# Performance work log

Measured on AMD Instinct MI355X. Metric: run time of the kernel, lower is better.

## Reference

```python
import jax, jax.numpy as jnp
import numpy as np

BUCKETS = 32
DIM = 1024
HEADS = 16
TEMP = 0.75
SINK_ITERS = 7
LOG_EPS = 1e-6
GUMBEL_EPS = 1e-4


def _sinkhorn(r, n_iters):
    # iterative row/col log-normalization, then exp (matches torch loop)
    for _ in range(n_iters):
        r = r - jax.scipy.special.logsumexp(r, axis=2, keepdims=True)
        r = r - jax.scipy.special.logsumexp(r, axis=1, keepdims=True)
    return jnp.exp(r)


def setup_inputs() -> dict:
    key = jax.random.key(0)
    kq, kk, kv, kw, kg = jax.random.split(key, 5)
    B, H, T, DH = 4, 16, 4096, 64
    q = jax.random.normal(kq, (B, H, T, DH), jnp.float32)
    k = jax.random.normal(kk, (B, H, T, DH), jnp.float32)
    v = jax.random.normal(kv, (B, H, T, DH), jnp.float32)
    sort_w = jax.random.normal(kw, (1, H, DH, BUCKETS), jnp.float32)
    u = jax.random.uniform(kg, (B * H, BUCKETS, BUCKETS), jnp.float32, 0.0, 1.0)
    gumbel_noise = -jnp.log(-jnp.log(u + GUMBEL_EPS) + GUMBEL_EPS)
    return {"q": q, "k": k, "v": v, "sort_w": sort_w, "gumbel_noise": gumbel_noise}


def reference(q, k, v, sort_w, gumbel_noise):
    b, h, t, dh = q.shape
    bh = b * h
    bsz = t // BUCKETS  # tokens per bucket
    # bucket: (bh, buckets, bsz, dh)
    qb = q.reshape(bh, BUCKETS, bsz, dh)
    kb = k.reshape(bh, BUCKETS, bsz, dh)
    vb = v.reshape(bh, BUCKETS, bsz, dh)
    # bucket summaries for routing
    b_k_r = kb.sum(axis=2)  # (bh, buckets, dh)
    e_w = jnp.broadcast_to(sort_w, (b, h, dh, BUCKETS)).reshape(bh, dh, BUCKETS)
    R = jnp.log(jax.nn.relu(jnp.einsum('bud,bdv->buv', b_k_r, e_w)) + LOG_EPS)
    R = (R + gumbel_noise) / TEMP
    R = _sinkhorn(R, SINK_ITERS)  # soft permutation matrix (bh, buckets, buckets)
    R = jnp.tril(R, -1)  # causal: only attend to strictly earlier buckets
    # soft-permute key/value buckets
    k_re = jnp.einsum('buv,bvtd->butd', R, kb)
    v_re = jnp.einsum('buv,bvtd->butd', R, vb)
    bk = jnp.concatenate([k_re, kb], axis=2)  # (bh, buckets, 2*bsz, dh)
    bv = jnp.concatenate([v_re, vb], axis=2)
    dots = jnp.einsum('buie,buje->buij', qb, bk) * (DIM ** -0.5)
    attn = jax.nn.softmax(dots, axis=-1)
    out = jnp.einsum('buij,buje->buie', attn, bv)  # (bh, buckets, bsz, dh)
    return out.reshape(b, h, t, dh)
```

## Files before the change

### kernel.cpp

```cpp
#include <hip/hip_runtime.h>
#include <hip/hip_bf16.h>

#define BUCKETS 32
#define BSZ 128
#define DH 64
#define TEMPINV 1.3333333333333333f
#define SINK_ITERS 7
#define LOG_EPS 1e-6f
#define SCALE 0.03125f

typedef short bf16x8 __attribute__((ext_vector_type(8)));
typedef float f32x4 __attribute__((ext_vector_type(4)));

__device__ __forceinline__ void bf8_to_f32(const uint4 x, float* f) {
    f[0] = __uint_as_float(x.x << 16);
    f[1] = __uint_as_float(x.x & 0xffff0000u);
    f[2] = __uint_as_float(x.y << 16);
    f[3] = __uint_as_float(x.y & 0xffff0000u);
    f[4] = __uint_as_float(x.z << 16);
    f[5] = __uint_as_float(x.z & 0xffff0000u);
    f[6] = __uint_as_float(x.w << 16);
    f[7] = __uint_as_float(x.w & 0xffff0000u);
}

__device__ __forceinline__ unsigned f2bf(float f) {
    unsigned x = __float_as_uint(f);
    return (x + 0x7fffu + ((x >> 16) & 1u)) >> 16;
}

__device__ __forceinline__ uint4 packbf8(const float* f) {
    uint4 r;
    r.x = f2bf(f[0]) | (f2bf(f[1]) << 16);
    r.y = f2bf(f[2]) | (f2bf(f[3]) << 16);
    r.z = f2bf(f[4]) | (f2bf(f[5]) << 16);
    r.w = f2bf(f[6]) | (f2bf(f[7]) << 16);
    return r;
}

__device__ __forceinline__ void load_lds16(const uint4* g, uint4* l) {
    __builtin_amdgcn_global_load_lds(
        (const __attribute__((address_space(1))) unsigned int*)g,
        (__attribute__((address_space(3))) unsigned int*)l, 16, 0, 0);
}

__global__ __launch_bounds__(256) void bksum_kernel(
    const float* __restrict__ kptr, float* __restrict__ bkr)
{
    const int t = blockIdx.x;
    const int tid = threadIdx.x;
    __shared__ float4 part[16][17];
    const float4* k4 = (const float4*)kptr + (size_t)t * 2048;
    const int c4 = tid & 15, rg = tid >> 4;
    float4 s; s.x = 0.f; s.y = 0.f; s.z = 0.f; s.w = 0.f;
    for (int r = rg; r < 128; r += 16) {
        float4 a = k4[r * 16 + c4];
        s.x += a.x; s.y += a.y; s.z += a.z; s.w += a.w;
    }
    part[rg][c4] = s;
    __syncthreads();
    if (tid < 16) {
        float4 acc = part[0][tid];
        for (int g = 1; g < 16; ++g) {
            float4 p = part[g][tid];
            acc.x += p.x; acc.y += p.y; acc.z += p.z; acc.w += p.w;
        }
        ((float4*)bkr)[t * 16 + tid] = acc;
    }
}

__global__ __launch_bounds__(256) void sinkhorn_kernel(
    const float* __restrict__ bkrp,
    const float* __restrict__ swptr,
    const float* __restrict__ gptr,
    float* __restrict__ Rout)
{
    const int b = blockIdx.x;
    const int h = b & 15;
    const int tid = threadIdx.x;

    __shared__ float bk[BUCKETS][DH];
    __shared__ float sw[DH][BUCKETS];
    __shared__ float R[BUCKETS][BUCKETS + 1];

    for (int o = tid; o < DH * BUCKETS; o += 256)
        sw[o >> 5][o & 31] = swptr[h * DH * BUCKETS + o];
    for (int o = tid; o < BUCKETS * DH; o += 256)
        bk[o >> 6][o & 63] = bkrp[b * 2048 + o];
    __syncthreads();

    for (int o = tid; o < BUCKETS * BUCKETS; o += 256) {
        const int uu = o >> 5, vv = o & 31;
        float dot = 0.f;
        for (int d = 0; d < DH; ++d) dot = fmaf(bk[uu][d], sw[d][vv], dot);
        const float g = gptr[b * 1024 + o];
        R[uu][vv] = (logf(fmaxf(dot, 0.f) + LOG_EPS) + g) * TEMPINV;
    }
    __syncthreads();

    const int rr = tid >> 3, sub = tid & 7;
    for (int it = 0; it < SINK_ITERS; ++it) {
        {
            float vals[4];
            float m = -1e30f, s = 0.f;
            #pragma unroll
            for (int q = 0; q < 4; ++q) { vals[q] = R[rr][sub * 4 + q]; m = fmaxf(m, vals[q]); }
            m = fmaxf(m, __shfl_xor(m, 1)); m = fmaxf(m, __shfl_xor(m, 2)); m = fmaxf(m, __shfl_xor(m, 4));
            #pragma unroll
            for (int q = 0; q < 4; ++q) s += expf(vals[q] - m);
            s += __shfl_xor(s, 1); s += __shfl_xor(s, 2); s += __shfl_xor(s, 4);
            const float lse = m + logf(s);
            #pragma unroll
            for (int q = 0; q < 4; ++q) R[rr][sub * 4 + q] = vals[q] - lse;
            __syncthreads();
        }
        {
            float vals[4];
            float m = -1e30f, s = 0.f;
            #pragma unroll
            for (int q = 0; q < 4; ++q) { vals[q] = R[sub * 4 + q][rr]; m = fmaxf(m, vals[q]); }
            m = fmaxf(m, __shfl_xor(m, 1)); m = fmaxf(m, __shfl_xor(m, 2)); m = fmaxf(m, __shfl_xor(m, 4));
            #pragma unroll
            for (int q = 0; q < 4; ++q) s += expf(vals[q] - m);
            s += __shfl_xor(s, 1); s += __shfl_xor(s, 2); s += __shfl_xor(s, 4);
            const float lse = m + logf(s);
            #pragma unroll
            for (int q = 0; q < 4; ++q) R[sub * 4 + q][rr] = vals[q] - lse;
            __syncthreads();
        }
    }

    for (int o = tid; o < BUCKETS * BUCKETS; o += 256) {
        const int uu = o >> 5, vv = o & 31;
        Rout[b * 1024 + o] = (vv < uu) ? expf(R[uu][vv]) : 0.f;
    }
}

__global__ __launch_bounds__(256, 4) void reshuffle3_kernel(
    const float* __restrict__ kptr,
    const float* __restrict__ vptr,
    const float* __restrict__ bkrp,
    const float* __restrict__ swptr,
    const float* __restrict__ gptr,
    uint4* __restrict__ kimg,
    uint4* __restrict__ vimg)
{
    const int j0 = blockIdx.x;
    const int b  = blockIdx.y;
    const int h  = b & 15;
    const int tid = threadIdx.x;
    const int u = tid >> 3, c8 = tid & 7;

    __shared__ float ls[32][4][64];
    __shared__ float lr[32][33];

    float* bk  = &ls[0][0][0];
    float* swl = bk + 2048;

    for (int o = tid; o < 2048; o += 256) bk[o]  = bkrp[b * 2048 + o];
    for (int o = tid; o < 2048; o += 256) swl[o] = swptr[h * 2048 + o];
    __syncthreads();
    for (int o = tid; o < 1024; o += 256) {
        const int uu = o >> 5, vv = o & 31;
        float dot = 0.f;
        for (int d = 0; d < 64; ++d) dot = fmaf(bk[uu * 64 + d], swl[d * 32 + vv], dot);
        lr[uu][vv] = (logf(fmaxf(dot, 0.f) + LOG_EPS) + gptr[b * 1024 + o]) * TEMPINV;
    }
    __syncthreads();

    const int rr = tid >> 3, sub = tid & 7;
    for (int it = 0; it < SINK_ITERS; ++it) {
        {
            float vals[4];
            float m = -1e30f, s = 0.f;
            #pragma unroll
            for (int q = 0; q < 4; ++q) { vals[q] = lr[rr][sub * 4 + q]; m = fmaxf(m, vals[q]); }
            m = fmaxf(m, __shfl_xor(m, 1)); m = fmaxf(m, __shfl_xor(m, 2)); m = fmaxf(m, __shfl_xor(m, 4));
            #pragma unroll
            for (int q = 0; q < 4; ++q) s += expf(vals[q] - m);
            s += __shfl_xor(s, 1); s += __shfl_xor(s, 2); s += __shfl_xor(s, 4);
            const float lse = m + logf(s);
            #pragma unroll
            for (int q = 0; q < 4; ++q) lr[rr][sub * 4 + q] = vals[q] - lse;
            __syncthreads();
        }
        {
            float vals[4];
            float m = -1e30f, s = 0.f;
            #pragma unroll
            for (int q = 0; q < 4; ++q) { vals[q] = lr[sub * 4 + q][rr]; m = fmaxf(m, vals[q]); }
            m = fmaxf(m, __shfl_xor(m, 1)); m = fmaxf(m, __shfl_xor(m, 2)); m = fmaxf(m, __shfl_xor(m, 4));
            #pragma unroll
            for (int q = 0; q < 4; ++q) s += expf(vals[q] - m);
            s += __shfl_xor(s, 1); s += __shfl_xor(s, 2); s += __shfl_xor(s, 4);
            const float lse = m + logf(s);
            #pragma unroll
            for (int q = 0; q < 4; ++q) lr[sub * 4 + q][rr] = vals[q] - lse;
            __syncthreads();
        }
    }
    for (int o = tid; o < 1024; o += 256) {
        const int uu = o >> 5, vv = o & 31;
        const float val = lr[uu][vv];
        lr[uu][vv] = (vv < uu) ? expf(val) : 0.f;
    }
    __syncthreads();

    float4* ls4 = (float4*)ls;

    {
        const float4* kb4 = (const float4*)kptr + (size_t)b * 65536 + j0 * 64;
        for (int it = 0; it < 8; ++it) {
            const int idx = it * 256 + tid;
            const int v = idx >> 6, i = idx & 63;
            ls4[v * 64 + i] = kb4[v * 2048 + i];
        }
    }
    __syncthreads();
    {
        float ka[4][8];
        #pragma unroll
        for (int r = 0; r < 4; ++r)
            #pragma unroll
            for (int t = 0; t < 8; ++t) ka[r][t] = 0.f;
        for (int vv = 0; vv < u; ++vv) {
            const float rwt = lr[u][vv];
            #pragma unroll
            for (int r = 0; r < 4; ++r)
                #pragma unroll
                for (int t = 0; t < 8; ++t)
                    ka[r][t] = fmaf(rwt, ls[vv][r][c8 * 8 + t], ka[r][t]);
        }
        uint4* kdst = kimg + ((size_t)b * 32 + u) * 2048;
        #pragma unroll
        for (int r = 0; r < 4; ++r) {
            const int j = j0 * 4 + r;
            kdst[j * 8 + (c8 ^ (j & 7))] = packbf8(ka[r]);
            float o8[8];
            #pragma unroll
            for (int t = 0; t < 8; ++t) o8[t] = ls[u][r][c8 * 8 + t];
            kdst[(128 + j) * 8 + (c8 ^ (j & 7))] = packbf8(o8);
        }
    }
    __syncthreads();

    {
        const float4* vb4 = (const float4*)vptr + (size_t)b * 65536 + j0 * 64;
        for (int it = 0; it < 8; ++it) {
            const int idx = it * 256 + tid;
            const int v = idx >> 6, i = idx & 63;
            ls4[v * 64 + i] = vb4[v * 2048 + i];
        }
    }
    __syncthreads();
    {
        float va[4][8];
        #pragma unroll
        for (int r = 0; r < 4; ++r)
            #pragma unroll
            for (int t = 0; t < 8; ++t) va[r][t] = 0.f;
        for (int vv = 0; vv < u; ++vv) {
            const float rwt = lr[u][vv];
            #pragma unroll
            for (int r = 0; r < 4; ++r)
                #pragma unroll
                for (int t = 0; t < 8; ++t)
                    va[r][t] = fmaf(rwt, ls[vv][r][c8 * 8 + t], va[r][t]);
        }
        uint2* vdst2 = (uint2*)(vimg + ((size_t)b * 32 + u) * 2048);
        const int p = j0 >> 1, half = j0 & 1;
        #pragma unroll
        for (int t = 0; t < 8; ++t) {
            const int blk = c8 * 8 + (t ^ c8);
            uint2 wre;
            wre.x = f2bf(va[0][t]) | (f2bf(va[1][t]) << 16);
            wre.y = f2bf(va[2][t]) | (f2bf(va[3][t]) << 16);
            vdst2[(p * 64 + blk) * 2 + half] = wre;
            uint2 wor;
            wor.x = f2bf(ls[u][0][c8 * 8 + t]) | (f2bf(ls[u][1][c8 * 8 + t]) << 16);
            wor.y = f2bf(ls[u][2][c8 * 8 + t]) | (f2bf(ls[u][3][c8 * 8 + t]) << 16);
            vdst2[((16 + p) * 64 + blk) * 2 + half] = wor;
        }
    }
}

__global__ __launch_bounds__(128) void attn_fallback(
    const float* __restrict__ qptr,
    const float* __restrict__ kptr,
    const float* __restrict__ vptr,
    const float* __restrict__ Rmat,
    float4* __restrict__ optr)
{
    const int u = blockIdx.x;
    const int b = blockIdx.y;
    const int tid = threadIdx.x;

    __shared__ uint4 sbk[2048];
    __shared__ uint4 sbv[2048];

    const float4* k4 = (const float4*)kptr + (size_t)b * 65536;
    const float4* v4 = (const float4*)vptr + (size_t)b * 65536;
    const float4* q4 = (const float4*)qptr + (size_t)b * 65536;

    const float* Rrow = Rmat + (b * BUCKETS + u) * BUCKETS;
    for (int o = tid; o < 1024; o += 128) {
        float ka[8] = {0.f,0.f,0.f,0.f,0.f,0.f,0.f,0.f};
        float va[8] = {0.f,0.f,0.f,0.f,0.f,0.f,0.f,0.f};
        for (int vv = 0; vv < u; ++vv) {
            const float r = Rrow[vv];
            float4 a = k4[vv * 2048 + 2 * o], c = k4[vv * 2048 + 2 * o + 1];
            ka[0] = fmaf(r, a.x, ka[0]); ka[1] = fmaf(r, a.y, ka[1]);
            ka[2] = fmaf(r, a.z, ka[2]); ka[3] = fmaf(r, a.w, ka[3]);
            ka[4] = fmaf(r, c.x, ka[4]); ka[5] = fmaf(r, c.y, ka[5]);
            ka[6] = fmaf(r, c.z, ka[6]); ka[7] = fmaf(r, c.w, ka[7]);
            float4 av = v4[vv * 2048 + 2 * o], cv = v4[vv * 2048 + 2 * o + 1];
            va[0] = fmaf(r, av.x, va[0]); va[1] = fmaf(r, av.y, va[1]);
            va[2] = fmaf(r, av.z, va[2]); va[3] = fmaf(r, av.w, va[3]);
            va[4] = fmaf(r, cv.x, va[4]); va[5] = fmaf(r, cv.y, va[5]);
            va[6] = fmaf(r, cv.z, va[6]); va[7] = fmaf(r, cv.w, va[7]);
        }
        sbk[o] = packbf8(ka);
        sbv[o] = packbf8(va);
        float4 a = k4[u * 2048 + 2 * o], c = k4[u * 2048 + 2 * o + 1];
        float f[8] = {a.x,a.y,a.z,a.w,c.x,c.y,c.z,c.w};
        sbk[1024 + o] = packbf8(f);
        float4 av = v4[u * 2048 + 2 * o], cv = v4[u * 2048 + 2 * o + 1];
        float g[8] = {av.x,av.y,av.z,av.w,cv.x,cv.y,cv.z,cv.w};
        sbv[1024 + o] = packbf8(g);
    }
    __syncthreads();

    const int i = tid;
    float qr[64];
    const float4* qrow = q4 + (u * 128 + i) * 16;
    for (int d4 = 0; d4 < 16; ++d4) {
        float4 t = qrow[d4];
        qr[d4 * 4 + 0] = t.x; qr[d4 * 4 + 1] = t.y;
        qr[d4 * 4 + 2] = t.z; qr[d4 * 4 + 3] = t.w;
    }

    float acc[64];
    for (int d = 0; d < 64; ++d) acc[d] = 0.f;
    float l = 0.f;

    for (int j = 0; j < 256; ++j) {
        float s = 0.f;
        for (int d8 = 0; d8 < 8; ++d8) {
            float f[8];
            bf8_to_f32(sbk[j * 8 + d8], f);
            for (int t = 0; t < 8; ++t) s = fmaf(qr[d8 * 8 + t], f[t], s);
        }
        const float p = __expf(s * SCALE);
        l += p;
        for (int d8 = 0; d8 < 8; ++d8) {
            float f[8];
            bf8_to_f32(sbv[j * 8 + d8], f);
            for (int t = 0; t < 8; ++t)
                acc[d8 * 8 + t] = fmaf(p, f[t], acc[d8 * 8 + t]);
        }
    }

    const float inv = 1.f / l;
    float4* orow = optr + (size_t)b * 65536 + (u * 128 + i) * 16;
    for (int d4 = 0; d4 < 16; ++d4) {
        float4 t;
        t.x = acc[d4 * 4 + 0] * inv;
        t.y = acc[d4 * 4 + 1] * inv;
        t.z = acc[d4 * 4 + 2] * inv;
        t.w = acc[d4 * 4 + 3] * inv;
        orow[d4] = t;
    }
}

__global__ __launch_bounds__(256) void attn_mfma2(
    const float* __restrict__ qptr,
    const uint4* __restrict__ kimg,
    const uint4* __restrict__ vimg,
    float* __restrict__ optr)
{
    const int u = blockIdx.x;
    const int b = blockIdx.y;
    const int tid = threadIdx.x;
    const int lane = tid & 63;
    const int w = tid >> 6;
    const int lg = lane >> 4;
    const int lr = lane & 15;

    __shared__ uint4 sK[2048];
    __shared__ uint4 sV[2048];
    __shared__ uint4 sP[1024];

    const size_t tile = (size_t)b * 32 + u;
    const uint4* gk = kimg + tile * 2048;
    const uint4* gv = vimg + tile * 2048;

    #pragma unroll
    for (int it = 0; it < 8; ++it)
        load_lds16(gk + it * 256 + tid, &sK[it * 256 + (w << 6)]);
    #pragma unroll
    for (int it = 0; it < 8; ++it)
        load_lds16(gv + it * 256 + tid, &sV[it * 256 + (w << 6)]);

    const float* qbase = qptr + (size_t)b * 262144 + (size_t)u * 8192;
    bf16x8 qf[2][2];
    #pragma unroll
    for (int mt = 0; mt < 2; ++mt)
        #pragma unroll
        for (int c = 0; c < 2; ++c) {
            const int row = w * 32 + mt * 16 + lr;
            const float4* qr = (const float4*)(qbase + row * 64 + (c * 4 + lg) * 8);
            float4 a = qr[0], cc = qr[1];
            float f[8] = {a.x * SCALE, a.y * SCALE, a.z * SCALE, a.w * SCALE,
                          cc.x * SCALE, cc.y * SCALE, cc.z * SCALE, cc.w * SCALE};
            uint4 tq = packbf8(f);
            qf[mt][c] = *(bf16x8*)&tq;
        }
    __syncthreads();

    uint4* sPw = sP + w * 256;
    unsigned short* sPh = (unsigned short*)sPw;

    f32x4 acc[2][4];
    float lsum[2][4];
    #pragma unroll
    for (int mt = 0; mt < 2; ++mt) {
        #pragma unroll
        for (int nt = 0; nt < 4; ++nt) {
            acc[mt][nt][0] = 0.f; acc[mt][nt][1] = 0.f;
            acc[mt][nt][2] = 0.f; acc[mt][nt][3] = 0.f;
        }
        #pragma unroll
        for (int r = 0; r < 4; ++r) lsum[mt][r] = 0.f;
    }

    for (int kb = 0; kb < 4; ++kb) {
        bf16x8 kf[4][2];
        #pragma unroll
        for (int nt = 0; nt < 4; ++nt)
            #pragma unroll
            for (int c = 0; c < 2; ++c) {
                const int j = kb * 64 + nt * 16 + lr;
                const int dcu = c * 4 + lg;
                uint4 t = sK[j * 8 + (dcu ^ (j & 7))];
                kf[nt][c] = *(bf16x8*)&t;
            }
        f32x4 s[2][4];
        #pragma unroll
        for (int mt = 0; mt < 2; ++mt)
            #pragma unroll
            for (int nt = 0; nt < 4; ++nt) {
                s[mt][nt][0] = 0.f; s[mt][nt][1] = 0.f;
                s[mt][nt][2] = 0.f; s[mt][nt][3] = 0.f;
            }
        __builtin_amdgcn_s_setprio(1);
        #pragma unroll
        for (int c = 0; c < 2; ++c)
            #pragma unroll
            for (int mt = 0; mt < 2; ++mt)
                #pragma unroll
                for (int nt = 0; nt < 4; ++nt)
                    s[mt][nt] = __builtin_amdgcn_mfma_f32_16x16x32_bf16(
                        qf[mt][c], kf[nt][c], s[mt][nt], 0, 0, 0);
        __builtin_amdgcn_s_setprio(0);

        #pragma unroll
        for (int mt = 0; mt < 2; ++mt)
            #pragma unroll
            for (int nt = 0; nt < 4; ++nt)
                #pragma unroll
                for (int r = 0; r < 4; ++r) {
                    const float p = __expf(s[mt][nt][r]);
                    lsum[mt][r] += p;
                    const int row = mt * 16 + lg * 4 + r;
                    const int col = nt * 16 + lr;
                    sPh[row * 64 + (((col >> 3) ^ (row & 7)) << 3) + (col & 7)] =
                        (unsigned short)f2bf(p);
                }
        asm volatile("s_waitcnt lgkmcnt(0)" ::: "memory");
        __builtin_amdgcn_sched_barrier(0);

        bf16x8 pf[2][2];
        #pragma unroll
        for (int mt = 0; mt < 2; ++mt)
            #pragma unroll
            for (int c = 0; c < 2; ++c) {
                const int row = mt * 16 + lr;
                const int dcu = c * 4 + lg;
                uint4 t = sPw[row * 8 + (dcu ^ (row & 7))];
                pf[mt][c] = *(bf16x8*)&t;
            }
        bf16x8 vf[4][2];
        #pragma unroll
        for (int nt = 0; nt < 4; ++nt)
            #pragma unroll
            for (int c = 0; c < 2; ++c) {
                const int p = kb * 8 + c * 4 + lg;
                const int d = nt * 16 + lr;
                const int blk = (d >> 3) * 8 + ((d & 7) ^ ((d >> 3) & 7));
                uint4 t = sV[p * 64 + blk];
                vf[nt][c] = *(bf16x8*)&t;
            }
        __builtin_amdgcn_s_setprio(1);
        #pragma unroll
        for (int c = 0; c < 2; ++c)
            #pragma unroll
            for (int mt = 0; mt < 2; ++mt)
                #pragma unroll
                for (int nt = 0; nt < 4; ++nt)
                    acc[mt][nt] = __builtin_amdgcn_mfma_f32_16x16x32_bf16(
                        pf[mt][c], vf[nt][c], acc[mt][nt], 0, 0, 0);
        __builtin_amdgcn_s_setprio(0);
    }

    #pragma unroll
    for (int mt = 0; mt < 2; ++mt)
        #pragma unroll
        for (int r = 0; r < 4; ++r) {
            float sum = lsum[mt][r];
            sum += __shfl_xor(sum, 1);
            sum += __shfl_xor(sum, 2);
            sum += __shfl_xor(sum, 4);
            sum += __shfl_xor(sum, 8);
            const float inv = 1.f / sum;
            const int row = mt * 16 + lg * 4 + r;
            float* orow = optr + (size_t)b * 262144 +
                          (size_t)(u * 128 + w * 32 + row) * 64;
            #pragma unroll
            for (int nt = 0; nt < 4; ++nt)
                orow[nt * 16 + lr] = acc[mt][nt][r] * inv;
        }
}

extern "C" void kernel_launch(void* const* d_in, const int* in_sizes, int n_in,
                              void* d_out, int out_size, void* d_ws, size_t ws_size,
                              hipStream_t stream) {
    const float* q  = (const float*)d_in[0];
    const float* k  = (const float*)d_in[1];
    const float* v  = (const float*)d_in[2];
    const float* sw = (const float*)d_in[3];
    const float* g  = (const float*)d_in[4];

    float* R    = (float*)d_ws;
    float* bkr  = (float*)((char*)d_ws + 262144);
    uint4* kimg = (uint4*)((char*)d_ws + 1048576);
    uint4* vimg = (uint4*)((char*)d_ws + 1048576 + 67108864);
    const bool big_ws = (ws_size >= (size_t)1048576 + 2u * 67108864u);

    bksum_kernel<<<dim3(2048), dim3(256), 0, stream>>>(k, bkr);
    if (big_ws) {
        reshuffle3_kernel<<<dim3(32, 64), dim3(256), 0, stream>>>(k, v, bkr, sw, g, kimg, vimg);
        attn_mfma2<<<dim3(32, 64), dim3(256), 0, stream>>>(q, kimg, vimg, (float*)d_out);
    } else {
        sinkhorn_kernel<<<dim3(64), dim3(256), 0, stream>>>(bkr, sw, g, R);
        attn_fallback<<<dim3(32, 64), dim3(128), 0, stream>>>(q, k, v, R, (float4*)d_out);
    }
}
```

Measured before the change: 340.4 us.

## Fuse bucket-sum into one Sinkhorn kernel and halve reshuffle grid

```diff
diff --git a/kernel.cpp b/kernel.cpp
--- a/kernel.cpp
+++ b/kernel.cpp
@@ -43,33 +43,8 @@
         (__attribute__((address_space(3))) unsigned int*)l, 16, 0, 0);
 }
 
-__global__ __launch_bounds__(256) void bksum_kernel(
-    const float* __restrict__ kptr, float* __restrict__ bkr)
-{
-    const int t = blockIdx.x;
-    const int tid = threadIdx.x;
-    __shared__ float4 part[16][17];
-    const float4* k4 = (const float4*)kptr + (size_t)t * 2048;
-    const int c4 = tid & 15, rg = tid >> 4;
-    float4 s; s.x = 0.f; s.y = 0.f; s.z = 0.f; s.w = 0.f;
-    for (int r = rg; r < 128; r += 16) {
-        float4 a = k4[r * 16 + c4];
-        s.x += a.x; s.y += a.y; s.z += a.z; s.w += a.w;
-    }
-    part[rg][c4] = s;
-    __syncthreads();
-    if (tid < 16) {
-        float4 acc = part[0][tid];
-        for (int g = 1; g < 16; ++g) {
-            float4 p = part[g][tid];
-            acc.x += p.x; acc.y += p.y; acc.z += p.z; acc.w += p.w;
-        }
-        ((float4*)bkr)[t * 16 + tid] = acc;
-    }
-}
-
-__global__ __launch_bounds__(256) void sinkhorn_kernel(
-    const float* __restrict__ bkrp,
+__global__ __launch_bounds__(1024) void sink_fused(
+    const float* __restrict__ kptr,
     const float* __restrict__ swptr,
     const float* __restrict__ gptr,
     float* __restrict__ Rout)
@@ -79,27 +54,35 @@
     const int tid = threadIdx.x;
 
     __shared__ float bk[BUCKETS][DH];
-    __shared__ float sw[DH][BUCKETS];
+    __shared__ float swl[DH][BUCKETS];
     __shared__ float R[BUCKETS][BUCKETS + 1];
 
-    for (int o = tid; o < DH * BUCKETS; o += 256)
-        sw[o >> 5][o & 31] = swptr[h * DH * BUCKETS + o];
-    for (int o = tid; o < BUCKETS * DH; o += 256)
-        bk[o >> 6][o & 63] = bkrp[b * 2048 + o];
+    {
+        const int u = tid >> 5, dp = tid & 31;
+        const float2* base = (const float2*)kptr + ((size_t)b * 32 + u) * 4096 + dp;
+        float sx = 0.f, sy = 0.f;
+        for (int t = 0; t < BSZ; ++t) {
+            const float2 a = base[t * 32];
+            sx += a.x; sy += a.y;
+        }
+        bk[u][dp * 2] = sx;
+        bk[u][dp * 2 + 1] = sy;
+    }
+    for (int o = tid; o < DH * BUCKETS; o += 1024)
+        swl[o >> 5][o & 31] = swptr[h * DH * BUCKETS + o];
     __syncthreads();
 
-    for (int o = tid; o < BUCKETS * BUCKETS; o += 256) {
-        const int uu = o >> 5, vv = o & 31;
+    {
+        const int uu = tid >> 5, vv = tid & 31;
         float dot = 0.f;
-        for (int d = 0; d < DH; ++d) dot = fmaf(bk[uu][d], sw[d][vv], dot);
-        const float g = gptr[b * 1024 + o];
-        R[uu][vv] = (logf(fmaxf(dot, 0.f) + LOG_EPS) + g) * TEMPINV;
+        for (int d = 0; d < DH; ++d) dot = fmaf(bk[uu][d], swl[d][vv], dot);
+        R[uu][vv] = (logf(fmaxf(dot, 0.f) + LOG_EPS) + gptr[b * 1024 + tid]) * TEMPINV;
     }
     __syncthreads();
 
     const int rr = tid >> 3, sub = tid & 7;
     for (int it = 0; it < SINK_ITERS; ++it) {
-        {
+        if (tid < 256) {
             float vals[4];
             float m = -1e30f, s = 0.f;
             #pragma unroll
@@ -111,9 +94,9 @@
             const float lse = m + logf(s);
             #pragma unroll
             for (int q = 0; q < 4; ++q) R[rr][sub * 4 + q] = vals[q] - lse;
-            __syncthreads();
-        }
-        {
+        }
+        __syncthreads();
+        if (tid < 256) {
             float vals[4];
             float m = -1e30f, s = 0.f;
             #pragma unroll
@@ -125,98 +108,47 @@
             const float lse = m + logf(s);
             #pragma unroll
             for (int q = 0; q < 4; ++q) R[sub * 4 + q][rr] = vals[q] - lse;
-            __syncthreads();
-        }
-    }
-
-    for (int o = tid; o < BUCKETS * BUCKETS; o += 256) {
-        const int uu = o >> 5, vv = o & 31;
-        Rout[b * 1024 + o] = (vv < uu) ? expf(R[uu][vv]) : 0.f;
-    }
-}
-
-__global__ __launch_bounds__(256, 4) void reshuffle3_kernel(
+        }
+        __syncthreads();
+    }
+
+    {
+        const int uu = tid >> 5, vv = tid & 31;
+        Rout[b * 1024 + tid] = (vv < uu) ? expf(R[uu][vv]) : 0.f;
+    }
+}
+
+__global__ __launch_bounds__(256, 4) void reshuffle5_kernel(
     const float* __restrict__ kptr,
     const float* __restrict__ vptr,
-    const float* __restrict__ bkrp,
-    const float* __restrict__ swptr,
-    const float* __restrict__ gptr,
+    const float* __restrict__ Rmat,
     uint4* __restrict__ kimg,
     uint4* __restrict__ vimg)
 {
     const int j0 = blockIdx.x;
     const int b  = blockIdx.y;
-    const int h  = b & 15;
     const int tid = threadIdx.x;
-    const int u = tid >> 3, c8 = tid & 7;
+    const int w = tid >> 6, g = (tid >> 3) & 7, c8 = tid & 7;
+    const int u = g * 4 + w;
 
     __shared__ float ls[32][4][64];
     __shared__ float lr[32][33];
 
-    float* bk  = &ls[0][0][0];
-    float* swl = bk + 2048;
-
-    for (int o = tid; o < 2048; o += 256) bk[o]  = bkrp[b * 2048 + o];
-    for (int o = tid; o < 2048; o += 256) swl[o] = swptr[h * 2048 + o];
-    __syncthreads();
-    for (int o = tid; o < 1024; o += 256) {
-        const int uu = o >> 5, vv = o & 31;
-        float dot = 0.f;
-        for (int d = 0; d < 64; ++d) dot = fmaf(bk[uu * 64 + d], swl[d * 32 + vv], dot);
-        lr[uu][vv] = (logf(fmaxf(dot, 0.f) + LOG_EPS) + gptr[b * 1024 + o]) * TEMPINV;
-    }
-    __syncthreads();
-
-    const int rr = tid >> 3, sub = tid & 7;
-    for (int it = 0; it < SINK_ITERS; ++it) {
-        {
-            float vals[4];
-            float m = -1e30f, s = 0.f;
-            #pragma unroll
-            for (int q = 0; q < 4; ++q) { vals[q] = lr[rr][sub * 4 + q]; m = fmaxf(m, vals[q]); }
-            m = fmaxf(m, __shfl_xor(m, 1)); m = fmaxf(m, __shfl_xor(m, 2)); m = fmaxf(m, __shfl_xor(m, 4));
-            #pragma unroll
-            for (int q = 0; q < 4; ++q) s += expf(vals[q] - m);
-            s += __shfl_xor(s, 1); s += __shfl_xor(s, 2); s += __shfl_xor(s, 4);
-            const float lse = m + logf(s);
-            #pragma unroll
-            for (int q = 0; q < 4; ++q) lr[rr][sub * 4 + q] = vals[q] - lse;
-            __syncthreads();
-        }
-        {
-            float vals[4];
-            float m = -1e30f, s = 0.f;
-            #pragma unroll
-            for (int q = 0; q < 4; ++q) { vals[q] = lr[sub * 4 + q][rr]; m = fmaxf(m, vals[q]); }
-            m = fmaxf(m, __shfl_xor(m, 1)); m = fmaxf(m, __shfl_xor(m, 2)); m = fmaxf(m, __shfl_xor(m, 4));
-            #pragma unroll
-            for (int q = 0; q < 4; ++q) s += expf(vals[q] - m);
-            s += __shfl_xor(s, 1); s += __shfl_xor(s, 2); s += __shfl_xor(s, 4);
-            const float lse = m + logf(s);
-            #pragma unroll
-            for (int q = 0; q < 4; ++q) lr[sub * 4 + q][rr] = vals[q] - lse;
-            __syncthreads();
-        }
-    }
-    for (int o = tid; o < 1024; o += 256) {
-        const int uu = o >> 5, vv = o & 31;
-        const float val = lr[uu][vv];
-        lr[uu][vv] = (vv < uu) ? expf(val) : 0.f;
-    }
-    __syncthreads();
+    for (int o = tid; o < 1024; o += 256)
+        lr[o >> 5][o & 31] = Rmat[b * 1024 + o];
 
     float4* ls4 = (float4*)ls;
-
-    {
-        const float4* kb4 = (const float4*)kptr + (size_t)b * 65536 + j0 * 64;
+    uint4* kdst = kimg + ((size_t)b * 32 + u) * 2048;
+
+    #pragma unroll
+    for (int q = 0; q < 2; ++q) {
+        const float4* kb4 = (const float4*)kptr + (size_t)b * 65536 + (j0 * 8 + q * 4) * 16;
         for (int it = 0; it < 8; ++it) {
             const int idx = it * 256 + tid;
             const int v = idx >> 6, i = idx & 63;
             ls4[v * 64 + i] = kb4[v * 2048 + i];
         }
-    }
-    __syncthreads();
-    {
+        __syncthreads();
         float ka[4][8];
         #pragma unroll
         for (int r = 0; r < 4; ++r)
@@ -230,29 +162,29 @@
                 for (int t = 0; t < 8; ++t)
                     ka[r][t] = fmaf(rwt, ls[vv][r][c8 * 8 + t], ka[r][t]);
         }
-        uint4* kdst = kimg + ((size_t)b * 32 + u) * 2048;
         #pragma unroll
         for (int r = 0; r < 4; ++r) {
-            const int j = j0 * 4 + r;
+            const int j = j0 * 8 + q * 4 + r;
             kdst[j * 8 + (c8 ^ (j & 7))] = packbf8(ka[r]);
             float o8[8];
             #pragma unroll
             for (int t = 0; t < 8; ++t) o8[t] = ls[u][r][c8 * 8 + t];
             kdst[(128 + j) * 8 + (c8 ^ (j & 7))] = packbf8(o8);
         }
-    }
-    __syncthreads();
-
-    {
-        const float4* vb4 = (const float4*)vptr + (size_t)b * 65536 + j0 * 64;
+        __syncthreads();
+    }
+
+    unsigned rex[8], rey[8], rez[8], rew[8];
+    unsigned orx[8], ory[8], orz[8], orw[8];
+    #pragma unroll
+    for (int q = 0; q < 2; ++q) {
+        const float4* vb4 = (const float4*)vptr + (size_t)b * 65536 + (j0 * 8 + q * 4) * 16;
         for (int it = 0; it < 8; ++it) {
             const int idx = it * 256 + tid;
             const int v = idx >> 6, i = idx & 63;
             ls4[v * 64 + i] = vb4[v * 2048 + i];
         }
-    }
-    __syncthreads();
-    {
+        __syncthreads();
         float va[4][8];
         #pragma unroll
         for (int r = 0; r < 4; ++r)
@@ -266,19 +198,34 @@
                 for (int t = 0; t < 8; ++t)
                     va[r][t] = fmaf(rwt, ls[vv][r][c8 * 8 + t], va[r][t]);
         }
-        uint2* vdst2 = (uint2*)(vimg + ((size_t)b * 32 + u) * 2048);
-        const int p = j0 >> 1, half = j0 & 1;
+        if (q == 0) {
+            #pragma unroll
+            for (int t = 0; t < 8; ++t) {
+                rex[t] = f2bf(va[0][t]) | (f2bf(va[1][t]) << 16);
+                rey[t] = f2bf(va[2][t]) | (f2bf(va[3][t]) << 16);
+                orx[t] = f2bf(ls[u][0][c8 * 8 + t]) | (f2bf(ls[u][1][c8 * 8 + t]) << 16);
+                ory[t] = f2bf(ls[u][2][c8 * 8 + t]) | (f2bf(ls[u][3][c8 * 8 + t]) << 16);
+            }
+        } else {
+            #pragma unroll
+            for (int t = 0; t < 8; ++t) {
+                rez[t] = f2bf(va[0][t]) | (f2bf(va[1][t]) << 16);
+                rew[t] = f2bf(va[2][t]) | (f2bf(va[3][t]) << 16);
+                orz[t] = f2bf(ls[u][0][c8 * 8 + t]) | (f2bf(ls[u][1][c8 * 8 + t]) << 16);
+                orw[t] = f2bf(ls[u][2][c8 * 8 + t]) | (f2bf(ls[u][3][c8 * 8 + t]) << 16);
+            }
+        }
+        __syncthreads();
+    }
+    {
+        uint4* vdst = vimg + ((size_t)b * 32 + u) * 2048;
         #pragma unroll
         for (int t = 0; t < 8; ++t) {
             const int blk = c8 * 8 + (t ^ c8);
-            uint2 wre;
-            wre.x = f2bf(va[0][t]) | (f2bf(va[1][t]) << 16);
-            wre.y = f2bf(va[2][t]) | (f2bf(va[3][t]) << 16);
-            vdst2[(p * 64 + blk) * 2 + half] = wre;
-            uint2 wor;
-            wor.x = f2bf(ls[u][0][c8 * 8 + t]) | (f2bf(ls[u][1][c8 * 8 + t]) << 16);
-            wor.y = f2bf(ls[u][2][c8 * 8 + t]) | (f2bf(ls[u][3][c8 * 8 + t]) << 16);
-            vdst2[((16 + p) * 64 + blk) * 2 + half] = wor;
+            uint4 wre; wre.x = rex[t]; wre.y = rey[t]; wre.z = rez[t]; wre.w = rew[t];
+            vdst[j0 * 64 + blk] = wre;
+            uint4 wor; wor.x = orx[t]; wor.y = ory[t]; wor.z = orz[t]; wor.w = orw[t];
+            vdst[(16 + j0) * 64 + blk] = wor;
         }
     }
 }
@@ -324,8 +271,8 @@
         float f[8] = {a.x,a.y,a.z,a.w,c.x,c.y,c.z,c.w};
         sbk[1024 + o] = packbf8(f);
         float4 av = v4[u * 2048 + 2 * o], cv = v4[u * 2048 + 2 * o + 1];
-        float g[8] = {av.x,av.y,av.z,av.w,cv.x,cv.y,cv.z,cv.w};
-        sbv[1024 + o] = packbf8(g);
+        float gg[8] = {av.x,av.y,av.z,av.w,cv.x,cv.y,cv.z,cv.w};
+        sbv[1024 + o] = packbf8(gg);
     }
     __syncthreads();
 
@@ -540,17 +487,15 @@
     const float* g  = (const float*)d_in[4];
 
     float* R    = (float*)d_ws;
-    float* bkr  = (float*)((char*)d_ws + 262144);
     uint4* kimg = (uint4*)((char*)d_ws + 1048576);
     uint4* vimg = (uint4*)((char*)d_ws + 1048576 + 67108864);
     const bool big_ws = (ws_size >= (size_t)1048576 + 2u * 67108864u);
 
-    bksum_kernel<<<dim3(2048), dim3(256), 0, stream>>>(k, bkr);
+    sink_fused<<<dim3(64), dim3(1024), 0, stream>>>(k, sw, g, R);
     if (big_ws) {
-        reshuffle3_kernel<<<dim3(32, 64), dim3(256), 0, stream>>>(k, v, bkr, sw, g, kimg, vimg);
+        reshuffle5_kernel<<<dim3(16, 64), dim3(256), 0, stream>>>(k, v, R, kimg, vimg);
         attn_mfma2<<<dim3(32, 64), dim3(256), 0, stream>>>(q, kimg, vimg, (float*)d_out);
     } else {
-        sinkhorn_kernel<<<dim3(64), dim3(256), 0, stream>>>(bkr, sw, g, R);
         attn_fallback<<<dim3(32, 64), dim3(128), 0, stream>>>(q, k, v, R, (float4*)d_out);
     }
 }
```

Result: no change. 339.0 us (-0.4%).
